# Kernel tuning notes

Measured on AMD Instinct MI355X. Metric: run time of the kernel, lower is better.

Reference implementation:

```python
import jax, jax.numpy as jnp
import numpy as np

N_NODES = 100000
N_EDGES = 3200000
IN_DIM = 128
OUT_DIM = 64
ITERS = 2


def setup_inputs() -> dict:
    key = jax.random.key(0)
    k1, k2, k3, k4, k5, k6 = jax.random.split(key, 6)
    feature = jax.random.normal(k1, (N_NODES, IN_DIM), dtype=jnp.float32)
    src = jax.random.randint(k2, (N_EDGES,), 0, N_NODES, dtype=jnp.int32)
    dst = jax.random.randint(k3, (N_EDGES,), 0, N_NODES, dtype=jnp.int32)
    # Kaiming-ish scaling for stability
    W_lin = jax.random.normal(k4, (IN_DIM, OUT_DIM), dtype=jnp.float32) / np.sqrt(IN_DIM)
    W_d1 = jax.random.normal(k5, (OUT_DIM, OUT_DIM), dtype=jnp.float32) / np.sqrt(OUT_DIM)
    W_d2 = jax.random.normal(k6, (OUT_DIM, OUT_DIM), dtype=jnp.float32) / np.sqrt(OUT_DIM)
    return {"feature": feature, "src": src, "dst": dst,
            "W_lin": W_lin, "W_d1": W_d1, "W_d2": W_d2}


def reference(feature, src, dst, W_lin, W_d1, W_d2):
    # u_i^0 = 0 ; u_i^j = tanh(linear(x_i) + dense(sum_{k in N(i)} u_k^{j-1}))
    base = feature @ W_lin                       # [N, OUT_DIM] (no bias)
    n = feature.shape[0]
    u = jnp.zeros((n, OUT_DIM), dtype=feature.dtype)
    for _ in range(ITERS):
        # copy_u + sum: message u[src] scattered-summed at dst
        m = jax.ops.segment_sum(u[src], dst, num_segments=n)   # [N, OUT_DIM]
        # Dense (2 layers, relu between, no bias): W_d2 @ relu(W_d1 @ m)
        h = jax.nn.relu(m @ W_d1) @ W_d2
        u = jnp.tanh(base + h)
    return u
```

## Files before the change

kernel.cpp:

```cpp
#include <hip/hip_runtime.h>
#include <math.h>

#define N_NODES 100000
#define N_EDGES 3200000
#define IN_DIM  128
#define OUT_DIM 64

#define BSHIFT   7
#define BNODES   128
#define NBUCKETS ((N_NODES + BNODES - 1) / BNODES)
#define NBINBLK  1024
#define CHUNK    (N_EDGES / NBINBLK)
#define SEGCAP   6144
#define MTILES   (N_NODES / 16)
#define GEMM_BLOCKS ((MTILES + 3) / 4)
#define RSTAGE   (SEGCAP / 512)

typedef _Float16 half8 __attribute__((ext_vector_type(8)));
typedef float    f32x4 __attribute__((ext_vector_type(4)));

__device__ __forceinline__ int xcd_swz(int i) {
    return (i & 7) * (NBINBLK / 8) + (i >> 3);
}

__device__ __forceinline__ void scan_btot(
    const int* __restrict__ Btot, int* bs, int* tmp)
{
    int t = threadIdx.x;
    const int C = (NBUCKETS + 511) / 512;
    int b0 = t * C;
    int s = 0;
#pragma unroll
    for (int i = 0; i < C; ++i) {
        int idx = b0 + i;
        int v = (idx < NBUCKETS) ? Btot[idx] : 0;
        if (idx < NBUCKETS) bs[idx] = v;
        s += v;
    }
    tmp[t] = s;
    __syncthreads();
#pragma unroll
    for (int o = 1; o < 512; o <<= 1) {
        int v = (t >= o) ? tmp[t - o] : 0;
        __syncthreads();
        tmp[t] += v;
        __syncthreads();
    }
    int excl = (t == 0) ? 0 : tmp[t - 1];
#pragma unroll
    for (int i = 0; i < C; ++i) {
        int idx = b0 + i;
        if (idx < NBUCKETS) { int v = bs[idx]; bs[idx] = excl; excl += v; }
    }
    __syncthreads();
}

__global__ __launch_bounds__(256) void fused_gemm_hist(
    const float* __restrict__ feature,
    const float* __restrict__ Wlin,
    float* __restrict__ base,
    _Float16* __restrict__ u1h,
    const int* __restrict__ dst,
    int* __restrict__ H)
{
    __shared__ int h[NBUCKETS];

    if (blockIdx.x < NBINBLK) {
        for (int k = threadIdx.x; k < NBUCKETS; k += 256) h[k] = 0;
        __syncthreads();

        int b = xcd_swz(blockIdx.x);
        int beg = b * CHUNK, end = beg + CHUNK;
        for (int i = beg + threadIdx.x; i < end; i += 256)
            atomicAdd(&h[dst[i] >> BSHIFT], 1);
        __syncthreads();

        for (int k = threadIdx.x; k < NBUCKETS; k += 256)
            H[(size_t)k * NBINBLK + b] = h[k];
        return;
    }

    int lane = threadIdx.x & 63;
    int wid  = ((blockIdx.x - NBINBLK) * 256 + threadIdx.x) >> 6;
    if (wid >= MTILES) return;

    int mrow = lane & 15;
    int kb   = lane >> 4;
    int k0   = kb * 8;

    half8 b[4][4];
#pragma unroll
    for (int s = 0; s < 4; ++s)
#pragma unroll
        for (int n = 0; n < 4; ++n)
#pragma unroll
            for (int j = 0; j < 8; ++j)
                b[s][n][j] = (_Float16)Wlin[(s * 32 + k0 + j) * OUT_DIM + n * 16 + mrow];

    int row = wid * 16 + mrow;
    const float4* fr = reinterpret_cast<const float4*>(feature + (size_t)row * IN_DIM);
    half8 a[4];
#pragma unroll
    for (int s = 0; s < 4; ++s) {
        float4 lo = fr[(s * 32 + k0) >> 2];
        float4 hi = fr[((s * 32 + k0) >> 2) + 1];
        a[s][0] = (_Float16)lo.x; a[s][1] = (_Float16)lo.y;
        a[s][2] = (_Float16)lo.z; a[s][3] = (_Float16)lo.w;
        a[s][4] = (_Float16)hi.x; a[s][5] = (_Float16)hi.y;
        a[s][6] = (_Float16)hi.z; a[s][7] = (_Float16)hi.w;
    }

    f32x4 acc[4];
#pragma unroll
    for (int n = 0; n < 4; ++n) acc[n] = (f32x4)0.f;

#pragma unroll
    for (int s = 0; s < 4; ++s)
#pragma unroll
        for (int n = 0; n < 4; ++n)
            acc[n] = __builtin_amdgcn_mfma_f32_16x16x32_f16(a[s], b[s][n], acc[n], 0, 0, 0);

#pragma unroll
    for (int n = 0; n < 4; ++n)
#pragma unroll
        for (int j = 0; j < 4; ++j) {
            int r = wid * 16 + kb * 4 + j;
            int c = n * 16 + mrow;
            float v = acc[n][j];
            base[(size_t)r * OUT_DIM + c] = v;
            u1h[(size_t)r * OUT_DIM + c] = (_Float16)tanhf(v);
        }
}

__global__ __launch_bounds__(NBINBLK) void scan_local(
    int* __restrict__ H, int* __restrict__ Btot)
{
    __shared__ int s[NBINBLK];
    int k = blockIdx.x, t = threadIdx.x;
    int v = H[(size_t)k * NBINBLK + t];
    s[t] = v;
    __syncthreads();
#pragma unroll
    for (int off = 1; off < NBINBLK; off <<= 1) {
        int x = (t >= off) ? s[t - off] : 0;
        __syncthreads();
        s[t] += x;
        __syncthreads();
    }
    H[(size_t)k * NBINBLK + t] = s[t] - v;
    if (t == NBINBLK - 1) Btot[k] = s[t];
}

__global__ __launch_bounds__(512) void bin_scatter(
    const int* __restrict__ src,
    const int* __restrict__ dst,
    const int* __restrict__ H,
    const int* __restrict__ Btot,
    int* __restrict__ ebuf)
{
    __shared__ int cur[NBUCKETS];
    __shared__ int bs[NBUCKETS];
    __shared__ int tmp[512];

    scan_btot(Btot, bs, tmp);

    int b = xcd_swz(blockIdx.x);
    for (int k = threadIdx.x; k < NBUCKETS; k += 512)
        cur[k] = H[(size_t)k * NBINBLK + b] + bs[k];
    __syncthreads();

    int beg = b * CHUNK, end = beg + CHUNK;
    for (int i = beg + threadIdx.x; i < end; i += 512) {
        int d = dst[i];
        int k = d >> BSHIFT;
        int p = atomicAdd(&cur[k], 1);
        ebuf[p] = src[i] | ((d & (BNODES - 1)) << 17);
    }
}

__global__ __launch_bounds__(512) void sort_gather(
    const int* __restrict__ Btot,
    const int* __restrict__ ebuf,
    const half8* __restrict__ u1v,
    half8* __restrict__ mh)
{
    __shared__ int seg[SEGCAP];
    __shared__ int cnt[BNODES];
    __shared__ int off[BNODES];
    __shared__ int st[BNODES + 1];
    __shared__ int bs[NBUCKETS];
    __shared__ int tmp[512];

    scan_btot(Btot, bs, tmp);

    int k = blockIdx.x;
    int beg = bs[k];
    int end = (k + 1 < NBUCKETS) ? bs[k + 1] : N_EDGES;
    int n = end - beg;

    for (int j = threadIdx.x; j < BNODES; j += 512) cnt[j] = 0;
    __syncthreads();

    int r[RSTAGE];
#pragma unroll
    for (int it = 0; it < RSTAGE; ++it) {
        int i = threadIdx.x + it * 512;
        int v = (i < n) ? ebuf[beg + i] : -1;
        r[it] = v;
        if (v >= 0) atomicAdd(&cnt[v >> 17], 1);
    }
    __syncthreads();

    if (threadIdx.x == 0) {
        int excl = 0;
        for (int j = 0; j < BNODES; ++j) {
            st[j] = excl; off[j] = excl; excl += cnt[j];
        }
        st[BNODES] = excl;
    }
    __syncthreads();

#pragma unroll
    for (int it = 0; it < RSTAGE; ++it) {
        int v = r[it];
        if (v >= 0) {
            int p = atomicAdd(&off[v >> 17], 1);
            seg[p] = v & 0x1FFFF;
        }
    }
    __syncthreads();

    int g = threadIdx.x >> 3;
    int c = threadIdx.x & 7;
    int node0 = k * BNODES;

#pragma unroll
    for (int half = 0; half < 2; ++half) {
        int j = g + half * 64;
        int node = node0 + j;
        if (node >= N_NODES) break;
        int eb = st[j], ee = st[j + 1];

        float acc[8];
#pragma unroll
        for (int i = 0; i < 8; ++i) acc[i] = 0.f;

        int e = eb;
        for (; e + 4 <= ee; e += 4) {
            int s0 = seg[e];
            int s1 = seg[e + 1];
            int s2 = seg[e + 2];
            int s3 = seg[e + 3];
            half8 a = u1v[(size_t)s0 * 8 + c];
            half8 b = u1v[(size_t)s1 * 8 + c];
            half8 gg = u1v[(size_t)s2 * 8 + c];
            half8 d = u1v[(size_t)s3 * 8 + c];
#pragma unroll
            for (int i = 0; i < 8; ++i)
                acc[i] += ((float)a[i] + (float)b[i]) + ((float)gg[i] + (float)d[i]);
        }
        for (; e < ee; ++e) {
            half8 a = u1v[(size_t)seg[e] * 8 + c];
#pragma unroll
            for (int i = 0; i < 8; ++i) acc[i] += (float)a[i];
        }

        half8 hv;
#pragma unroll
        for (int i = 0; i < 8; ++i) hv[i] = (_Float16)acc[i];
        mh[(size_t)node * 8 + c] = hv;
    }
}

__global__ __launch_bounds__(256) void dense_tanh(
    const half8* __restrict__ mh,
    const float* __restrict__ W1,
    const float* __restrict__ W2,
    const float* __restrict__ base,
    float* __restrict__ out)
{
    __shared__ _Float16 tl[4][16][72];
    int lane = threadIdx.x & 63;
    int w    = threadIdx.x >> 6;
    int wid  = (blockIdx.x * 256 + threadIdx.x) >> 6;
    if (wid >= MTILES) return;

    int mrow = lane & 15;
    int kb   = lane >> 4;
    int k0   = kb * 8;

    half8 b1[2][4], b2[2][4];
#pragma unroll
    for (int s = 0; s < 2; ++s)
#pragma unroll
        for (int n = 0; n < 4; ++n)
#pragma unroll
            for (int j = 0; j < 8; ++j) {
                b1[s][n][j] = (_Float16)W1[(s * 32 + k0 + j) * 64 + n * 16 + mrow];
                b2[s][n][j] = (_Float16)W2[(s * 32 + k0 + j) * 64 + n * 16 + mrow];
            }

    int row = wid * 16 + mrow;
    half8 a[2];
#pragma unroll
    for (int s = 0; s < 2; ++s)
        a[s] = mh[(size_t)row * 8 + ((s * 32 + k0) >> 3)];

    f32x4 acc1[4];
#pragma unroll
    for (int n = 0; n < 4; ++n) acc1[n] = (f32x4)0.f;
#pragma unroll
    for (int s = 0; s < 2; ++s)
#pragma unroll
        for (int n = 0; n < 4; ++n)
            acc1[n] = __builtin_amdgcn_mfma_f32_16x16x32_f16(a[s], b1[s][n], acc1[n], 0, 0, 0);

#pragma unroll
    for (int n = 0; n < 4; ++n)
#pragma unroll
        for (int j = 0; j < 4; ++j)
            tl[w][kb * 4 + j][n * 16 + mrow] = (_Float16)fmaxf(acc1[n][j], 0.f);

    half8 a2[2];
#pragma unroll
    for (int s = 0; s < 2; ++s)
        a2[s] = *reinterpret_cast<const half8*>(&tl[w][mrow][s * 32 + k0]);

    f32x4 acc2[4];
#pragma unroll
    for (int n = 0; n < 4; ++n) acc2[n] = (f32x4)0.f;
#pragma unroll
    for (int s = 0; s < 2; ++s)
#pragma unroll
        for (int n = 0; n < 4; ++n)
            acc2[n] = __builtin_amdgcn_mfma_f32_16x16x32_f16(a2[s], b2[s][n], acc2[n], 0, 0, 0);

#pragma unroll
    for (int n = 0; n < 4; ++n)
#pragma unroll
        for (int j = 0; j < 4; ++j) {
            int r = wid * 16 + kb * 4 + j;
            int c = n * 16 + mrow;
            out[(size_t)r * 64 + c] = tanhf(base[(size_t)r * 64 + c] + acc2[n][j]);
        }
}

extern "C" void kernel_launch(void* const* d_in, const int* in_sizes, int n_in,
                              void* d_out, int out_size, void* d_ws, size_t ws_size,
                              hipStream_t stream)
{
    const float* feature = (const float*)d_in[0];
    const int*   src     = (const int*)d_in[1];
    const int*   dst     = (const int*)d_in[2];
    const float* W_lin   = (const float*)d_in[3];
    const float* W_d1    = (const float*)d_in[4];
    const float* W_d2    = (const float*)d_in[5];
    float* out = (float*)d_out;

    const size_t NODE_F = (size_t)N_NODES * OUT_DIM;

    float*    base     = (float*)d_ws;
    _Float16* u1h      = (_Float16*)(base + NODE_F);
    _Float16* mh       = u1h + NODE_F;
    int*      H        = (int*)(mh + NODE_F);
    int*      Btot     = H + ((size_t)NBUCKETS * NBINBLK + 4);
    int*      ebuf     = Btot + (NBUCKETS + 4);

    fused_gemm_hist<<<NBINBLK + GEMM_BLOCKS, 256, 0, stream>>>(
        feature, W_lin, base, u1h, dst, H);

    scan_local<<<NBUCKETS, NBINBLK, 0, stream>>>(H, Btot);
    bin_scatter<<<NBINBLK, 512, 0, stream>>>(src, dst, H, Btot, ebuf);
    sort_gather<<<NBUCKETS, 512, 0, stream>>>(
        Btot, ebuf, (const half8*)u1h, (half8*)mh);

    dense_tanh<<<GEMM_BLOCKS, 256, 0, stream>>>(
        (const half8*)mh, W_d1, W_d2, base, out);
}
```

Before: 140.5 us.

## Fuse neighbor gather with dense MLP and tanh in one kernel

Merges the sort/gather kernel and the dense_tanh kernel. Each bucket block now writes its 128 aggregated rows into a shared-memory tile, then its 8 waves run the two MFMA layers plus tanh on them, reusing the dead seg buffer as relu scratch. This removes the global round trip of the fp16 message buffer and one kernel launch. In exchange, each block uses more LDS, which may lower occupancy in the gather phase, and each block reloads the weight matrices.

```diff
diff --git a/kernel.cpp b/kernel.cpp
--- a/kernel.cpp
+++ b/kernel.cpp
@@ -178,13 +178,17 @@
     }
 }
 
-__global__ __launch_bounds__(512) void sort_gather(
+__global__ __launch_bounds__(512) void sort_gather_dense(
     const int* __restrict__ Btot,
     const int* __restrict__ ebuf,
     const half8* __restrict__ u1v,
-    half8* __restrict__ mh)
+    const float* __restrict__ W1,
+    const float* __restrict__ W2,
+    const float* __restrict__ base,
+    float* __restrict__ out)
 {
     __shared__ int seg[SEGCAP];
+    __shared__ _Float16 m_tile[128 * 72];
     __shared__ int cnt[BNODES];
     __shared__ int off[BNODES];
     __shared__ int st[BNODES + 1];
@@ -197,6 +201,7 @@
     int beg = bs[k];
     int end = (k + 1 < NBUCKETS) ? bs[k + 1] : N_EDGES;
     int n = end - beg;
+    int node0 = k * BNODES;
 
     for (int j = threadIdx.x; j < BNODES; j += 512) cnt[j] = 0;
     __syncthreads();
@@ -230,119 +235,115 @@
     }
     __syncthreads();
 
-    int g = threadIdx.x >> 3;
-    int c = threadIdx.x & 7;
-    int node0 = k * BNODES;
-
-#pragma unroll
-    for (int half = 0; half < 2; ++half) {
-        int j = g + half * 64;
-        int node = node0 + j;
-        if (node >= N_NODES) break;
-        int eb = st[j], ee = st[j + 1];
-
-        float acc[8];
-#pragma unroll
-        for (int i = 0; i < 8; ++i) acc[i] = 0.f;
-
-        int e = eb;
-        for (; e + 4 <= ee; e += 4) {
-            int s0 = seg[e];
-            int s1 = seg[e + 1];
-            int s2 = seg[e + 2];
-            int s3 = seg[e + 3];
-            half8 a = u1v[(size_t)s0 * 8 + c];
-            half8 b = u1v[(size_t)s1 * 8 + c];
-            half8 gg = u1v[(size_t)s2 * 8 + c];
-            half8 d = u1v[(size_t)s3 * 8 + c];
-#pragma unroll
-            for (int i = 0; i < 8; ++i)
-                acc[i] += ((float)a[i] + (float)b[i]) + ((float)gg[i] + (float)d[i]);
+    {
+        int g = threadIdx.x >> 3;
+        int c = threadIdx.x & 7;
+
+#pragma unroll
+        for (int half = 0; half < 2; ++half) {
+            int j = g + half * 64;
+            int node = node0 + j;
+            if (node >= N_NODES) break;
+            int eb = st[j], ee = st[j + 1];
+
+            float acc[8];
+#pragma unroll
+            for (int i = 0; i < 8; ++i) acc[i] = 0.f;
+
+            int e = eb;
+            for (; e + 4 <= ee; e += 4) {
+                int s0 = seg[e];
+                int s1 = seg[e + 1];
+                int s2 = seg[e + 2];
+                int s3 = seg[e + 3];
+                half8 a = u1v[(size_t)s0 * 8 + c];
+                half8 b = u1v[(size_t)s1 * 8 + c];
+                half8 gg = u1v[(size_t)s2 * 8 + c];
+                half8 d = u1v[(size_t)s3 * 8 + c];
+#pragma unroll
+                for (int i = 0; i < 8; ++i)
+                    acc[i] += ((float)a[i] + (float)b[i]) + ((float)gg[i] + (float)d[i]);
+            }
+            for (; e < ee; ++e) {
+                half8 a = u1v[(size_t)seg[e] * 8 + c];
+#pragma unroll
+                for (int i = 0; i < 8; ++i) acc[i] += (float)a[i];
+            }
+
+            half8 hv;
+#pragma unroll
+            for (int i = 0; i < 8; ++i) hv[i] = (_Float16)acc[i];
+            *reinterpret_cast<half8*>(&m_tile[j * 72 + c * 8]) = hv;
         }
-        for (; e < ee; ++e) {
-            half8 a = u1v[(size_t)seg[e] * 8 + c];
-#pragma unroll
-            for (int i = 0; i < 8; ++i) acc[i] += (float)a[i];
-        }
-
-        half8 hv;
-#pragma unroll
-        for (int i = 0; i < 8; ++i) hv[i] = (_Float16)acc[i];
-        mh[(size_t)node * 8 + c] = hv;
-    }
-}
-
-__global__ __launch_bounds__(256) void dense_tanh(
-    const half8* __restrict__ mh,
-    const float* __restrict__ W1,
-    const float* __restrict__ W2,
-    const float* __restrict__ base,
-    float* __restrict__ out)
-{
-    __shared__ _Float16 tl[4][16][72];
-    int lane = threadIdx.x & 63;
-    int w    = threadIdx.x >> 6;
-    int wid  = (blockIdx.x * 256 + threadIdx.x) >> 6;
-    if (wid >= MTILES) return;
-
-    int mrow = lane & 15;
-    int kb   = lane >> 4;
-    int k0   = kb * 8;
-
-    half8 b1[2][4], b2[2][4];
-#pragma unroll
-    for (int s = 0; s < 2; ++s)
-#pragma unroll
-        for (int n = 0; n < 4; ++n)
-#pragma unroll
-            for (int j = 0; j < 8; ++j) {
-                b1[s][n][j] = (_Float16)W1[(s * 32 + k0 + j) * 64 + n * 16 + mrow];
-                b2[s][n][j] = (_Float16)W2[(s * 32 + k0 + j) * 64 + n * 16 + mrow];
+    }
+    __syncthreads();
+
+    {
+        int lane = threadIdx.x & 63;
+        int w    = threadIdx.x >> 6;
+        int mrow = lane & 15;
+        int kb   = lane >> 4;
+        int k0   = kb * 8;
+        _Float16* tlw = reinterpret_cast<_Float16*>(seg) + w * 16 * 72;
+
+        half8 b1[2][4], b2[2][4];
+#pragma unroll
+        for (int s = 0; s < 2; ++s)
+#pragma unroll
+            for (int nn = 0; nn < 4; ++nn)
+#pragma unroll
+                for (int j = 0; j < 8; ++j) {
+                    b1[s][nn][j] = (_Float16)W1[(s * 32 + k0 + j) * 64 + nn * 16 + mrow];
+                    b2[s][nn][j] = (_Float16)W2[(s * 32 + k0 + j) * 64 + nn * 16 + mrow];
+                }
+
+        half8 a[2];
+#pragma unroll
+        for (int s = 0; s < 2; ++s)
+            a[s] = *reinterpret_cast<const half8*>(
+                &m_tile[(w * 16 + mrow) * 72 + s * 32 + k0]);
+
+        f32x4 acc1[4];
+#pragma unroll
+        for (int nn = 0; nn < 4; ++nn) acc1[nn] = (f32x4)0.f;
+#pragma unroll
+        for (int s = 0; s < 2; ++s)
+#pragma unroll
+            for (int nn = 0; nn < 4; ++nn)
+                acc1[nn] = __builtin_amdgcn_mfma_f32_16x16x32_f16(a[s], b1[s][nn], acc1[nn], 0, 0, 0);
+
+#pragma unroll
+        for (int nn = 0; nn < 4; ++nn)
+#pragma unroll
+            for (int j = 0; j < 4; ++j)
+                tlw[(kb * 4 + j) * 72 + nn * 16 + mrow] = (_Float16)fmaxf(acc1[nn][j], 0.f);
+
+        half8 a2[2];
+#pragma unroll
+        for (int s = 0; s < 2; ++s)
+            a2[s] = *reinterpret_cast<const half8*>(&tlw[mrow * 72 + s * 32 + k0]);
+
+        f32x4 acc2[4];
+#pragma unroll
+        for (int nn = 0; nn < 4; ++nn) acc2[nn] = (f32x4)0.f;
+#pragma unroll
+        for (int s = 0; s < 2; ++s)
+#pragma unroll
+            for (int nn = 0; nn < 4; ++nn)
+                acc2[nn] = __builtin_amdgcn_mfma_f32_16x16x32_f16(a2[s], b2[s][nn], acc2[nn], 0, 0, 0);
+
+#pragma unroll
+        for (int nn = 0; nn < 4; ++nn)
+#pragma unroll
+            for (int j = 0; j < 4; ++j) {
+                int rr = node0 + w * 16 + kb * 4 + j;
+                if (rr < N_NODES) {
+                    int c = nn * 16 + mrow;
+                    out[(size_t)rr * 64 + c] =
+                        tanhf(base[(size_t)rr * 64 + c] + acc2[nn][j]);
+                }
             }
-
-    int row = wid * 16 + mrow;
-    half8 a[2];
-#pragma unroll
-    for (int s = 0; s < 2; ++s)
-        a[s] = mh[(size_t)row * 8 + ((s * 32 + k0) >> 3)];
-
-    f32x4 acc1[4];
-#pragma unroll
-    for (int n = 0; n < 4; ++n) acc1[n] = (f32x4)0.f;
-#pragma unroll
-    for (int s = 0; s < 2; ++s)
-#pragma unroll
-        for (int n = 0; n < 4; ++n)
-            acc1[n] = __builtin_amdgcn_mfma_f32_16x16x32_f16(a[s], b1[s][n], acc1[n], 0, 0, 0);
-
-#pragma unroll
-    for (int n = 0; n < 4; ++n)
-#pragma unroll
-        for (int j = 0; j < 4; ++j)
-            tl[w][kb * 4 + j][n * 16 + mrow] = (_Float16)fmaxf(acc1[n][j], 0.f);
-
-    half8 a2[2];
-#pragma unroll
-    for (int s = 0; s < 2; ++s)
-        a2[s] = *reinterpret_cast<const half8*>(&tl[w][mrow][s * 32 + k0]);
-
-    f32x4 acc2[4];
-#pragma unroll
-    for (int n = 0; n < 4; ++n) acc2[n] = (f32x4)0.f;
-#pragma unroll
-    for (int s = 0; s < 2; ++s)
-#pragma unroll
-        for (int n = 0; n < 4; ++n)
-            acc2[n] = __builtin_amdgcn_mfma_f32_16x16x32_f16(a2[s], b2[s][n], acc2[n], 0, 0, 0);
-
-#pragma unroll
-    for (int n = 0; n < 4; ++n)
-#pragma unroll
-        for (int j = 0; j < 4; ++j) {
-            int r = wid * 16 + kb * 4 + j;
-            int c = n * 16 + mrow;
-            out[(size_t)r * 64 + c] = tanhf(base[(size_t)r * 64 + c] + acc2[n][j]);
-        }
+    }
 }
 
 extern "C" void kernel_launch(void* const* d_in, const int* in_sizes, int n_in,
@@ -361,8 +362,7 @@
 
     float*    base     = (float*)d_ws;
     _Float16* u1h      = (_Float16*)(base + NODE_F);
-    _Float16* mh       = u1h + NODE_F;
-    int*      H        = (int*)(mh + NODE_F);
+    int*      H        = (int*)(u1h + NODE_F);
     int*      Btot     = H + ((size_t)NBUCKETS * NBINBLK + 4);
     int*      ebuf     = Btot + (NBUCKETS + 4);
 
@@ -371,9 +371,6 @@
 
     scan_local<<<NBUCKETS, NBINBLK, 0, stream>>>(H, Btot);
     bin_scatter<<<NBINBLK, 512, 0, stream>>>(src, dst, H, Btot, ebuf);
-    sort_gather<<<NBUCKETS, 512, 0, stream>>>(
-        Btot, ebuf, (const half8*)u1h, (half8*)mh);
-
-    dense_tanh<<<GEMM_BLOCKS, 256, 0, stream>>>(
-        (const half8*)mh, W_d1, W_d2, base, out);
-}
+    sort_gather_dense<<<NBUCKETS, 512, 0, stream>>>(
+        Btot, ebuf, (const half8*)u1h, W_d1, W_d2, base, out);
+}
```

New measurement: 143.6 us. +2.2%, slower.
